# Kernel tuning notes

Measured on AMD Instinct MI355X. Metric: run time of the kernel, lower is better.

## Reference

```python
import jax, jax.numpy as jnp
import numpy as np

D_MODEL, N_HEADS, D_STATE, N_GROUPS, CHUNK = 2048, 32, 64, 1, 256
BATCH, SEQLEN = 2, 4096


def setup_inputs() -> dict:
    key = jax.random.key(0)
    ks = jax.random.split(key, 8)
    s = 0.02
    d, h, n, g = D_MODEL, N_HEADS, D_STATE, N_GROUPS
    return {
        "x": jax.random.normal(ks[0], (BATCH, SEQLEN, d), jnp.float32),
        "A_log": jnp.log(jnp.arange(1, h + 1, dtype=jnp.float32)),
        "D": jnp.ones((h,), jnp.float32),
        "B_w": jax.random.normal(ks[1], (g * n, d), jnp.float32) * s,
        "B_b": jnp.zeros((g * n,), jnp.float32),
        "C_w": jax.random.normal(ks[2], (g * n, d), jnp.float32) * s,
        "C_b": jnp.zeros((g * n,), jnp.float32),
        "dt_w": jax.random.normal(ks[3], (h, d), jnp.float32) * s,
        "dt_b": jnp.zeros((h,), jnp.float32),
        "out_w": jax.random.normal(ks[4], (d, d), jnp.float32) * s,
        "out_b": jnp.zeros((d,), jnp.float32),
    }


def segsum(v):
    # v: [..., T] -> [..., T, T]; out[i,j] = sum_{k=j+1..i} v[k] for i>=j, -inf else
    cs = jnp.cumsum(v, axis=-1)
    seg = cs[..., :, None] - cs[..., None, :]
    T = v.shape[-1]
    mask = jnp.tril(jnp.ones((T, T), bool))
    return jnp.where(mask, seg, -jnp.inf)


def _ssd(x, A_log, D, B_w, B_b, C_w, C_b, dt_w, dt_b, out_w, out_b):
    b, t, d = x.shape
    h = A_log.shape[0]
    n = B_w.shape[0] // N_GROUPS
    p = d // h
    l = CHUNK
    c = t // l

    A = -jnp.exp(A_log.astype(jnp.float32))                      # [h]
    B = (x @ B_w.T + B_b).reshape(b, t, N_GROUPS, n)             # g=1
    C = (x @ C_w.T + C_b).reshape(b, t, N_GROUPS, n)
    B = jnp.broadcast_to(B, (b, t, h, n))                        # repeat groups -> heads
    C = jnp.broadcast_to(C, (b, t, h, n))
    dt = jax.nn.softplus(x @ dt_w.T + dt_b)                      # [b,t,h]
    xh = x.reshape(b, t, h, p)

    # chunked SSD (Mamba2 mamba_chunk_scan_combined math)
    xc = xh.reshape(b, c, l, h, p)
    Bc = B.reshape(b, c, l, h, n)
    Cc = C.reshape(b, c, l, h, n)
    dtc = dt.reshape(b, c, l, h)
    dA = jnp.transpose(dtc * A, (0, 3, 1, 2))                    # [b,h,c,l]
    A_cumsum = jnp.cumsum(dA, axis=-1)                           # [b,h,c,l]

    # 1. intra-chunk (diagonal blocks)
    L = jnp.exp(segsum(dA))                                      # [b,h,c,l,l]
    xdt = xc * dtc[..., None]                                    # [b,c,l,h,p]
    Y_diag = jnp.einsum('bclhn,bcshn,bhcls,bcshp->bclhp', Cc, Bc, L, xdt)

    # 2. per-chunk final states
    decay_states = jnp.exp(A_cumsum[..., -1:] - A_cumsum)        # [b,h,c,l]
    states = jnp.einsum('bclhn,bhcl,bclhp->bchpn', Bc, decay_states, xdt)

    # 3. inter-chunk recurrence on chunk states
    states = jnp.concatenate([jnp.zeros_like(states[:, :1]), states], axis=1)  # [b,c+1,h,p,n]
    dA_last = jnp.pad(A_cumsum[..., -1], ((0, 0), (0, 0), (1, 0)))             # [b,h,c+1]
    decay_chunk = jnp.exp(segsum(dA_last))                                     # [b,h,c+1,c+1]
    new_states = jnp.einsum('bhzc,bchpn->bzhpn', decay_chunk, states)
    prev_states = new_states[:, :-1]                                           # [b,c,h,p,n]

    # 4. state -> output contribution
    state_decay_out = jnp.exp(A_cumsum)                          # [b,h,c,l]
    Y_off = jnp.einsum('bclhn,bchpn,bhcl->bclhp', Cc, prev_states, state_decay_out)

    Y = (Y_diag + Y_off).reshape(b, t, h, p) + D[None, None, :, None] * xh
    return Y.reshape(b, t, d) @ out_w.T + out_b


def reference(x, A_log, D, B_w, B_b, C_w, C_b, dt_w, dt_b, out_w, out_b):
    return _ssd(x, A_log, D, B_w, B_b, C_w, C_b, dt_w, dt_b, out_w, out_b)
```

## Files before the change

kernel.cpp:

```cpp
#include <hip/hip_runtime.h>
#include <hip/hip_bf16.h>
#include <math.h>

namespace {
constexpr int kDModel = 2048;
constexpr int kHeads  = 32;
constexpr int kState  = 64;
constexpr int kP      = 64;
constexpr int kChunk  = 256;
constexpr int kNChunk = 16;
constexpr int kBatch  = 2;
constexpr int kSeq    = 4096;
constexpr int kM      = kBatch * kSeq;
}

typedef __bf16 bf16_t;
typedef __attribute__((ext_vector_type(8))) __bf16 bf16x8;
typedef __attribute__((ext_vector_type(4))) __bf16 bf16x4;
typedef __attribute__((ext_vector_type(4))) float f32x4;

__device__ __forceinline__ void gload_lds16(const void* g, void* l) {
    __builtin_amdgcn_global_load_lds(
        (const __attribute__((address_space(1))) void*)g,
        (__attribute__((address_space(3))) void*)l,
        16, 0, 0);
}

__global__ __launch_bounds__(256)
void gemm_bcdt(const bf16_t* __restrict__ A, const bf16_t* __restrict__ W,
               const float* __restrict__ b0, const float* __restrict__ b1,
               const float* __restrict__ b2,
               bf16_t* __restrict__ o0h, bf16_t* __restrict__ o1h,
               float* __restrict__ o2f)
{
    constexpr int K = kDModel;
    __shared__ __bf16 AstS[64 * 32];
    __shared__ __bf16 WstS[128 * 32];
    const int tid  = threadIdx.x;
    const int lane = tid & 63;
    const int wave = tid >> 6;
    const int wm = (wave >> 1) * 32;
    const int wn = (wave & 1) * 64;
    const int l15 = lane & 15, quad = lane >> 4;
    const int m0 = blockIdx.y * 64;
    const int n0 = blockIdx.x * 128;
    const int u0 = tid, u1 = tid + 256;

    f32x4 acc[2][4];
    #pragma unroll
    for (int i = 0; i < 2; ++i)
        #pragma unroll
        for (int j = 0; j < 4; ++j)
            acc[i][j] = (f32x4){0.f, 0.f, 0.f, 0.f};

    for (int k0 = 0; k0 < K; k0 += 32) {
        gload_lds16(A + (size_t)(m0 + (tid >> 2)) * K + k0 + (tid & 3) * 8, AstS + tid * 8);
        gload_lds16(W + (size_t)(n0 + (u0 >> 2)) * K + k0 + (u0 & 3) * 8, WstS + u0 * 8);
        gload_lds16(W + (size_t)(n0 + (u1 >> 2)) * K + k0 + (u1 & 3) * 8, WstS + u1 * 8);
        __syncthreads();
        bf16x8 af[2], bfr[4];
        #pragma unroll
        for (int mi = 0; mi < 2; ++mi)
            af[mi] = *reinterpret_cast<const bf16x8*>(&AstS[(wm + mi * 16 + l15) * 32 + quad * 8]);
        #pragma unroll
        for (int ni = 0; ni < 4; ++ni)
            bfr[ni] = *reinterpret_cast<const bf16x8*>(&WstS[(wn + ni * 16 + l15) * 32 + quad * 8]);
        #pragma unroll
        for (int mi = 0; mi < 2; ++mi)
            #pragma unroll
            for (int ni = 0; ni < 4; ++ni)
                acc[mi][ni] = __builtin_amdgcn_mfma_f32_16x16x32_bf16(
                    af[mi], bfr[ni], acc[mi][ni], 0, 0, 0);
        __syncthreads();
    }

    #pragma unroll
    for (int mi = 0; mi < 2; ++mi) {
        #pragma unroll
        for (int reg = 0; reg < 4; ++reg) {
            const int r = m0 + wm + mi * 16 + quad * 4 + reg;
            #pragma unroll
            for (int ni = 0; ni < 4; ++ni) {
                const float v = acc[mi][ni][reg];
                const int n = n0 + wn + ni * 16 + l15;
                if (n < 64) {
                    o0h[(size_t)r * 64 + n] = (bf16_t)(v + b0[n]);
                } else if (n < 128) {
                    o1h[(size_t)r * 64 + (n - 64)] = (bf16_t)(v + b1[n - 64]);
                } else if (n < 160) {
                    float z = v + b2[n - 128];
                    o2f[(size_t)r * 32 + (n - 128)] = (z > 20.f) ? z : log1pf(expf(z));
                }
            }
        }
    }
}

__global__ __launch_bounds__(512, 2)
void gemm256_out(const bf16_t* __restrict__ Ap, const bf16_t* __restrict__ Bp,
                 const float* __restrict__ bias, float* __restrict__ C)
{
    constexpr int M = 8192, N = 2048, NT = 2048 / 32;
    __shared__ __bf16 Ab[3][4 * 256 * 8];
    __shared__ __bf16 Bb[3][4 * 256 * 8];
    const int tid  = threadIdx.x;
    const int lane = tid & 63;
    const int wave = tid >> 6;
    const int l15 = lane & 15, quad = lane >> 4;
    const int bid = blockIdx.x;
    const int mt = (bid & 7) * 4 + ((bid >> 3) & 3);
    const int nt = bid >> 5;
    const int m0 = mt * 256;
    const int n0 = nt * 256;
    const int wm = (wave >> 2) * 128;
    const int wn = (wave & 3) * 64;

    const int u0 = tid, u1 = tid + 512;
    auto stage = [&](int t2, int stb) {
        const int ks0 = t2 * 4;
        const bf16_t* As = Ap + ((size_t)ks0 * M + m0) * 8;
        const bf16_t* Bs = Bp + ((size_t)ks0 * N + n0) * 8;
        __bf16* Al = &Ab[stb][0];
        __bf16* Bl = &Bb[stb][0];
        gload_lds16(As + ((size_t)(u0 >> 8) * M + (u0 & 255)) * 8, Al + u0 * 8);
        gload_lds16(As + ((size_t)(u1 >> 8) * M + (u1 & 255)) * 8, Al + u1 * 8);
        gload_lds16(Bs + ((size_t)(u0 >> 8) * N + (u0 & 255)) * 8, Bl + u0 * 8);
        gload_lds16(Bs + ((size_t)(u1 >> 8) * N + (u1 & 255)) * 8, Bl + u1 * 8);
    };

    f32x4 acc[8][4];
    #pragma unroll
    for (int i = 0; i < 8; ++i)
        #pragma unroll
        for (int j = 0; j < 4; ++j)
            acc[i][j] = (f32x4){0.f, 0.f, 0.f, 0.f};

    stage(0, 0);
    stage(1, 1);
    asm volatile("s_waitcnt vmcnt(4)" ::: "memory");
    __builtin_amdgcn_s_barrier();

    int cur = 0;
    for (int t = 0; t < NT; ++t) {
        const __bf16* Ac = &Ab[cur][0];
        const __bf16* Bc = &Bb[cur][0];
        int stb = cur + 2; if (stb >= 3) stb -= 3;

        bf16x8 af[4], bfr[4];
        #pragma unroll
        for (int mi = 0; mi < 4; ++mi)
            af[mi] = *reinterpret_cast<const bf16x8*>(
                &Ac[(quad * 256 + wm + mi * 16 + l15) * 8]);
        #pragma unroll
        for (int nj = 0; nj < 4; ++nj)
            bfr[nj] = *reinterpret_cast<const bf16x8*>(
                &Bc[(quad * 256 + wn + nj * 16 + l15) * 8]);
        if (t < NT - 2) stage(t + 2, stb);
        __builtin_amdgcn_s_setprio(1);
        #pragma unroll
        for (int mi = 0; mi < 4; ++mi)
            #pragma unroll
            for (int nj = 0; nj < 4; ++nj)
                acc[mi][nj] = __builtin_amdgcn_mfma_f32_16x16x32_bf16(
                    af[mi], bfr[nj], acc[mi][nj], 0, 0, 0);
        __builtin_amdgcn_s_setprio(0);

        #pragma unroll
        for (int mi = 0; mi < 4; ++mi)
            af[mi] = *reinterpret_cast<const bf16x8*>(
                &Ac[(quad * 256 + wm + 64 + mi * 16 + l15) * 8]);
        __builtin_amdgcn_s_setprio(1);
        #pragma unroll
        for (int mi = 0; mi < 4; ++mi)
            #pragma unroll
            for (int nj = 0; nj < 4; ++nj)
                acc[4 + mi][nj] = __builtin_amdgcn_mfma_f32_16x16x32_bf16(
                    af[mi], bfr[nj], acc[4 + mi][nj], 0, 0, 0);
        __builtin_amdgcn_s_setprio(0);

        if (t < NT - 2) {
            asm volatile("s_waitcnt vmcnt(4)" ::: "memory");
        } else if (t < NT - 1) {
            asm volatile("s_waitcnt vmcnt(0)" ::: "memory");
        }
        if (t < NT - 1) __builtin_amdgcn_s_barrier();
        cur = cur + 1; if (cur == 3) cur = 0;
    }

    float bia[4];
    #pragma unroll
    for (int nj = 0; nj < 4; ++nj) bia[nj] = bias[n0 + wn + nj * 16 + l15];
    #pragma unroll
    for (int mi = 0; mi < 8; ++mi) {
        #pragma unroll
        for (int reg = 0; reg < 4; ++reg) {
            const int r = m0 + wm + mi * 16 + quad * 4 + reg;
            #pragma unroll
            for (int nj = 0; nj < 4; ++nj) {
                const int c = n0 + wn + nj * 16 + l15;
                C[(size_t)r * N + c] = acc[mi][nj][reg] + bia[nj];
            }
        }
    }
}

__global__ __launch_bounds__(256)
void cvt_bf16_kernel(const float* __restrict__ src, bf16_t* __restrict__ dst, int n)
{
    const int i = (blockIdx.x * 256 + threadIdx.x) * 4;
    if (i + 3 < n) {
        const float4 v = *reinterpret_cast<const float4*>(src + i);
        dst[i + 0] = (bf16_t)v.x;
        dst[i + 1] = (bf16_t)v.y;
        dst[i + 2] = (bf16_t)v.z;
        dst[i + 3] = (bf16_t)v.w;
    }
}

__global__ __launch_bounds__(256)
void pack_wob_kernel(const float* __restrict__ W, bf16_t* __restrict__ Wp)
{
    const int idx = blockIdx.x * 256 + threadIdx.x;
    const int n = idx >> 8, ks = idx & 255;
    const float4 v0 = *reinterpret_cast<const float4*>(W + (size_t)n * 2048 + ks * 8);
    const float4 v1 = *reinterpret_cast<const float4*>(W + (size_t)n * 2048 + ks * 8 + 4);
    bf16x8 o;
    o[0] = (__bf16)v0.x; o[1] = (__bf16)v0.y; o[2] = (__bf16)v0.z; o[3] = (__bf16)v0.w;
    o[4] = (__bf16)v1.x; o[5] = (__bf16)v1.y; o[6] = (__bf16)v1.z; o[7] = (__bf16)v1.w;
    *reinterpret_cast<bf16x8*>(Wp + ((size_t)ks * 2048 + n) * 8) = o;
}

__global__ __launch_bounds__(256)
void pack_w_kernel(const float* __restrict__ B_w, const float* __restrict__ C_w,
                   const float* __restrict__ dt_w, bf16_t* __restrict__ wcat)
{
    const int idx = blockIdx.x * 256 + threadIdx.x;
    const int r = idx >> 11, k = idx & 2047;
    float v = 0.f;
    if (r < 64)       v = B_w[r * 2048 + k];
    else if (r < 128) v = C_w[(r - 64) * 2048 + k];
    else if (r < 160) v = dt_w[(r - 128) * 2048 + k];
    wcat[idx] = (bf16_t)v;
}

__global__ __launch_bounds__(kChunk)
void dtcumsum_kernel(const float* __restrict__ dtm, const float* __restrict__ A_log,
                     float* __restrict__ Acs)
{
    const int blk = blockIdx.x;
    const int ci = blk & (kNChunk - 1);
    const int hi = (blk >> 4) & (kHeads - 1);
    const int bi = blk >> 9;
    const int t = threadIdx.x;
    const float Ah = -expf(A_log[hi]);
    __shared__ float s[kChunk];
    s[t] = dtm[((size_t)bi * kSeq + ci * kChunk + t) * kHeads + hi] * Ah;
    __syncthreads();
    for (int off = 1; off < kChunk; off <<= 1) {
        const float add = (t >= off) ? s[t - off] : 0.f;
        __syncthreads();
        s[t] += add;
        __syncthreads();
    }
    Acs[((size_t)(bi * kHeads + hi) * kNChunk + ci) * kChunk + t] = s[t];
}

__global__ __launch_bounds__(256)
void bT_kernel(const bf16_t* __restrict__ Bb16, bf16_t* __restrict__ bTg)
{
    const int ci = blockIdx.x & (kNChunk - 1);
    const int bi = blockIdx.x >> 4;
    const size_t rowbase = (size_t)bi * kSeq + ci * kChunk;
    __shared__ __bf16 T[64 * 264];
    const int tid = threadIdx.x;
    bf16x8 v[8];
    #pragma unroll
    for (int e = 0; e < 8; ++e)
        v[e] = *reinterpret_cast<const bf16x8*>(Bb16 + (rowbase + tid) * 64 + e * 8);
    #pragma unroll
    for (int e = 0; e < 8; ++e)
        #pragma unroll
        for (int j = 0; j < 8; ++j)
            T[(e * 8 + j) * 264 + tid] = v[e][j];
    __syncthreads();
    const int n = tid >> 2, seg = (tid & 3) * 64;
    bf16_t* dst = bTg + ((size_t)(bi * kNChunk + ci)) * (64 * 256) + n * 256 + seg;
    #pragma unroll
    for (int j = 0; j < 8; ++j) {
        *reinterpret_cast<bf16x8*>(dst + j * 8) =
            *reinterpret_cast<const bf16x8*>(&T[n * 264 + seg + j * 8]);
    }
}

__global__ __launch_bounds__(256)
void xdtT_kernel(const bf16_t* __restrict__ xb, const float* __restrict__ dtm,
                 bf16_t* __restrict__ xdtT)
{
    const int blk = blockIdx.x;
    const int hi = blk & (kHeads - 1);
    const int ci = (blk >> 5) & (kNChunk - 1);
    const int bi = blk >> 9;
    const size_t rowbase = (size_t)bi * kSeq + ci * kChunk;
    __shared__ __bf16 T[64 * 264];
    const int tid = threadIdx.x;
    const float d = dtm[(rowbase + tid) * kHeads + hi];
    bf16x8 v[8];
    #pragma unroll
    for (int e = 0; e < 8; ++e)
        v[e] = *reinterpret_cast<const bf16x8*>(xb + (rowbase + tid) * kDModel + hi * kP + e * 8);
    #pragma unroll
    for (int e = 0; e < 8; ++e)
        #pragma unroll
        for (int j = 0; j < 8; ++j)
            T[(e * 8 + j) * 264 + tid] = (__bf16)((float)v[e][j] * d);
    __syncthreads();
    const int p = tid >> 2, seg = (tid & 3) * 64;
    bf16_t* dst = xdtT + (size_t)blk * (64 * 256) + p * 256 + seg;
    #pragma unroll
    for (int j = 0; j < 8; ++j) {
        *reinterpret_cast<bf16x8*>(dst + j * 8) =
            *reinterpret_cast<const bf16x8*>(&T[p * 264 + seg + j * 8]);
    }
}

__global__ __launch_bounds__(256)
void states_mfma(const bf16_t* __restrict__ xdtT, const bf16_t* __restrict__ bTg,
                 const float* __restrict__ Acs, float* __restrict__ states)
{
    const int blk = blockIdx.x;
    const int hi = blk & (kHeads - 1);
    const int ci = (blk >> 5) & (kNChunk - 1);
    const int bi = blk >> 9;
    __shared__ __bf16 Xa[64 * 264];
    __shared__ __bf16 Bt[64 * 264];
    __shared__ float dec[kChunk];
    const int tid = threadIdx.x;
    const int lane = tid & 63;
    const int wave = tid >> 6;
    const int l15 = lane & 15, quad = lane >> 4;

    const float* acs = Acs + ((size_t)(bi * kHeads + hi) * kNChunk + ci) * kChunk;
    dec[tid] = expf(acs[kChunk - 1] - acs[tid]);
    __syncthreads();

    const bf16_t* bsrc = bTg + ((size_t)(bi * kNChunk + ci)) * (64 * 256);
    const bf16_t* xsrc = xdtT + (size_t)blk * (64 * 256);
    #pragma unroll
    for (int e = 0; e < 8; ++e) {
        const int u = e * 256 + tid;
        const int r = u >> 5, seg = (u & 31) * 8;
        *reinterpret_cast<bf16x8*>(&Bt[r * 264 + seg]) =
            *reinterpret_cast<const bf16x8*>(bsrc + r * 256 + seg);
        bf16x8 xv = *reinterpret_cast<const bf16x8*>(xsrc + r * 256 + seg);
        bf16x8 xo;
        #pragma unroll
        for (int j = 0; j < 8; ++j)
            xo[j] = (__bf16)((float)xv[j] * dec[seg + j]);
        *reinterpret_cast<bf16x8*>(&Xa[r * 264 + seg]) = xo;
    }
    __syncthreads();

    f32x4 acc[4];
    #pragma unroll
    for (int ni = 0; ni < 4; ++ni) acc[ni] = (f32x4){0.f, 0.f, 0.f, 0.f};
    #pragma unroll
    for (int kk = 0; kk < 8; ++kk) {
        const bf16x8 af = *reinterpret_cast<const bf16x8*>(
            &Xa[(wave * 16 + l15) * 264 + kk * 32 + quad * 8]);
        #pragma unroll
        for (int ni = 0; ni < 4; ++ni) {
            const bf16x8 bf = *reinterpret_cast<const bf16x8*>(
                &Bt[(ni * 16 + l15) * 264 + kk * 32 + quad * 8]);
            acc[ni] = __builtin_amdgcn_mfma_f32_16x16x32_bf16(af, bf, acc[ni], 0, 0, 0);
        }
    }
    float* sp = states + (size_t)blk * (kP * kState);
    #pragma unroll
    for (int reg = 0; reg < 4; ++reg) {
        const int p = wave * 16 + quad * 4 + reg;
        #pragma unroll
        for (int ni = 0; ni < 4; ++ni)
            sp[(size_t)p * kState + ni * 16 + l15] = acc[ni][reg];
    }
}

__global__ __launch_bounds__(256)
void chunkscan_kernel(const float* __restrict__ states, const float* __restrict__ Acs,
                      float* __restrict__ prevs)
{
    const int q  = blockIdx.x & 15;
    const int hi = (blockIdx.x >> 4) & (kHeads - 1);
    const int bi = blockIdx.x >> 9;
    const int e  = q * 256 + threadIdx.x;
    __shared__ float ea[kNChunk];
    if (threadIdx.x < kNChunk)
        ea[threadIdx.x] = expf(Acs[((size_t)(bi * kHeads + hi) * kNChunk + threadIdx.x)
                                   * kChunk + kChunk - 1]);
    __syncthreads();
    float P = 0.f;
    prevs[((size_t)(bi * kNChunk + 0) * kHeads + hi) * (kP * kState) + e] = 0.f;
    for (int c = 1; c < kNChunk; ++c) {
        P = fmaf(ea[c - 1], P,
                 states[((size_t)(bi * kNChunk + (c - 1)) * kHeads + hi) * (kP * kState) + e]);
        prevs[((size_t)(bi * kNChunk + c) * kHeads + hi) * (kP * kState) + e] = P;
    }
}

__global__ __launch_bounds__(256)
void ychunk_mfma(const float* __restrict__ x, const bf16_t* __restrict__ Bb16,
                 const bf16_t* __restrict__ Cb16, const bf16_t* __restrict__ xdtT,
                 const float* __restrict__ Acs, const float* __restrict__ prevs,
                 const float* __restrict__ Dvec, bf16_t* __restrict__ Yp)
{
    const int blk = blockIdx.x;
    const int lt = blk & 3;
    const int hi = (blk >> 2) & (kHeads - 1);
    const int ci = (blk >> 7) & (kNChunk - 1);
    const int bi = blk >> 11;
    __shared__ float acs_s[kChunk];
    __shared__ __bf16 Cs[64 * 72];
    __shared__ __bf16 Bs[64 * 72];
    __shared__ __bf16 Xt[64 * 72];
    __shared__ __bf16 Sp[64 * 72];
    const int tid = threadIdx.x;
    const int lane = tid & 63;
    const int wave = tid >> 6;
    const int l15 = lane & 15, quad = lane >> 4;
    const size_t rowbase = (size_t)bi * kSeq + ci * kChunk;
    const bf16_t* xdsrc = xdtT + ((size_t)((bi * kNChunk + ci) * kHeads + hi)) * (64 * 256);

    acs_s[tid] = Acs[((size_t)(bi * kHeads + hi) * kNChunk + ci) * kChunk + tid];
    #pragma unroll
    for (int e = 0; e < 2; ++e) {
        const int u = e * 256 + tid;
        const int r = u >> 3, seg = (u & 7) * 8;
        *reinterpret_cast<bf16x8*>(&Cs[r * 72 + seg]) =
            *reinterpret_cast<const bf16x8*>(Cb16 + (rowbase + lt * 64 + r) * 64 + seg);
    }
    const float* pp = prevs + ((size_t)(bi * kNChunk + ci) * kHeads + hi) * (kP * kState);
    #pragma unroll
    for (int e = 0; e < 4; ++e) {
        const int idx = e * 1024 + tid * 4;
        const int r = idx >> 6, c = idx & 63;
        const float4 vp = *reinterpret_cast<const float4*>(pp + idx);
        bf16x4 p4;
        p4[0] = (__bf16)vp.x; p4[1] = (__bf16)vp.y;
        p4[2] = (__bf16)vp.z; p4[3] = (__bf16)vp.w;
        *reinterpret_cast<bf16x4*>(&Bs[r * 72 + c]) = p4;
    }
    __syncthreads();

    bf16x8 af[2];
    af[0] = *reinterpret_cast<const bf16x8*>(&Cs[(wave * 16 + l15) * 72 + quad * 8]);
    af[1] = *reinterpret_cast<const bf16x8*>(&Cs[(wave * 16 + l15) * 72 + 32 + quad * 8]);

    f32x4 yacc[4];
    #pragma unroll
    for (int ni = 0; ni < 4; ++ni) yacc[ni] = (f32x4){0.f, 0.f, 0.f, 0.f};
    #pragma unroll
    for (int ni = 0; ni < 4; ++ni) {
        const bf16x8 b0 = *reinterpret_cast<const bf16x8*>(&Bs[(ni * 16 + l15) * 72 + quad * 8]);
        const bf16x8 b1 = *reinterpret_cast<const bf16x8*>(&Bs[(ni * 16 + l15) * 72 + 32 + quad * 8]);
        yacc[ni] = __builtin_amdgcn_mfma_f32_16x16x32_bf16(af[0], b0, yacc[ni], 0, 0, 0);
        yacc[ni] = __builtin_amdgcn_mfma_f32_16x16x32_bf16(af[1], b1, yacc[ni], 0, 0, 0);
    }
    const int mrow = wave * 16 + quad * 4;
    {
        float es[4];
        #pragma unroll
        for (int reg = 0; reg < 4; ++reg) es[reg] = expf(acs_s[lt * 64 + mrow + reg]);
        #pragma unroll
        for (int ni = 0; ni < 4; ++ni)
            #pragma unroll
            for (int reg = 0; reg < 4; ++reg) yacc[ni][reg] *= es[reg];
    }

    for (int st = 0; st <= lt; ++st) {
        __syncthreads();
        #pragma unroll
        for (int e = 0; e < 2; ++e) {
            const int u = e * 256 + tid;
            const int r = u >> 3, seg = (u & 7) * 8;
            *reinterpret_cast<bf16x8*>(&Bs[r * 72 + seg]) =
                *reinterpret_cast<const bf16x8*>(Bb16 + (rowbase + st * 64 + r) * 64 + seg);
            *reinterpret_cast<bf16x8*>(&Xt[r * 72 + seg]) =
                *reinterpret_cast<const bf16x8*>(xdsrc + r * 256 + st * 64 + seg);
        }
        __syncthreads();
        f32x4 sacc[4];
        #pragma unroll
        for (int ni = 0; ni < 4; ++ni) sacc[ni] = (f32x4){0.f, 0.f, 0.f, 0.f};
        #pragma unroll
        for (int ni = 0; ni < 4; ++ni) {
            const bf16x8 b0 = *reinterpret_cast<const bf16x8*>(&Bs[(ni * 16 + l15) * 72 + quad * 8]);
            const bf16x8 b1 = *reinterpret_cast<const bf16x8*>(&Bs[(ni * 16 + l15) * 72 + 32 + quad * 8]);
            sacc[ni] = __builtin_amdgcn_mfma_f32_16x16x32_bf16(af[0], b0, sacc[ni], 0, 0, 0);
            sacc[ni] = __builtin_amdgcn_mfma_f32_16x16x32_bf16(af[1], b1, sacc[ni], 0, 0, 0);
        }
        #pragma unroll
        for (int reg = 0; reg < 4; ++reg) {
            const int l = lt * 64 + mrow + reg;
            const float al = acs_s[l];
            #pragma unroll
            for (int ni = 0; ni < 4; ++ni) {
                const int scol = ni * 16 + l15;
                const int sg = st * 64 + scol;
                float v = sacc[ni][reg] * expf(al - acs_s[sg]);
                if (st == lt && sg > l) v = 0.f;
                Sp[(mrow + reg) * 72 + scol] = (__bf16)v;
            }
        }
        __syncthreads();
        const bf16x8 as0 = *reinterpret_cast<const bf16x8*>(&Sp[(wave * 16 + l15) * 72 + quad * 8]);
        const bf16x8 as1 = *reinterpret_cast<const bf16x8*>(&Sp[(wave * 16 + l15) * 72 + 32 + quad * 8]);
        #pragma unroll
        for (int ni = 0; ni < 4; ++ni) {
            const bf16x8 x0 = *reinterpret_cast<const bf16x8*>(&Xt[(ni * 16 + l15) * 72 + quad * 8]);
            const bf16x8 x1 = *reinterpret_cast<const bf16x8*>(&Xt[(ni * 16 + l15) * 72 + 32 + quad * 8]);
            yacc[ni] = __builtin_amdgcn_mfma_f32_16x16x32_bf16(as0, x0, yacc[ni], 0, 0, 0);
            yacc[ni] = __builtin_amdgcn_mfma_f32_16x16x32_bf16(as1, x1, yacc[ni], 0, 0, 0);
        }
    }

    const float Dh = Dvec[hi];
    #pragma unroll
    for (int reg = 0; reg < 4; ++reg) {
        const size_t tg = rowbase + lt * 64 + mrow + reg;
        #pragma unroll
        for (int ni = 0; ni < 4; ++ni) {
            const int p = ni * 16 + l15;
            const float v = yacc[ni][reg] + Dh * x[tg * kDModel + hi * kP + p];
            Yp[((size_t)(hi * 8 + (p >> 3)) * (size_t)kM + tg) * 8 + (p & 7)] = (bf16_t)v;
        }
    }
}

extern "C" void kernel_launch(void* const* d_in, const int* in_sizes, int n_in,
                              void* d_out, int out_size, void* d_ws, size_t ws_size,
                              hipStream_t stream)
{
    (void)in_sizes; (void)n_in; (void)out_size; (void)ws_size;
    const float* x     = (const float*)d_in[0];
    const float* A_log = (const float*)d_in[1];
    const float* Dvec  = (const float*)d_in[2];
    const float* B_w   = (const float*)d_in[3];
    const float* B_b   = (const float*)d_in[4];
    const float* C_w   = (const float*)d_in[5];
    const float* C_b   = (const float*)d_in[6];
    const float* dt_w  = (const float*)d_in[7];
    const float* dt_b  = (const float*)d_in[8];
    const float* out_w = (const float*)d_in[9];
    const float* out_b = (const float*)d_in[10];
    float* out = (float*)d_out;

    float* ws = (float*)d_ws;
    float* dtm    = ws;
    float* Acs    = dtm + (size_t)kM * kHeads;
    float* states = Acs + (size_t)kBatch * kHeads * kNChunk * kChunk;
    float* prevs  = states + (size_t)kBatch * kNChunk * kHeads * kP * kState;
    bf16_t* xb    = (bf16_t*)(prevs + (size_t)kBatch * kNChunk * kHeads * kP * kState);
    bf16_t* Y     = xb;
    bf16_t* Bb16  = xb + (size_t)kM * kDModel;
    bf16_t* Cb16  = Bb16 + (size_t)kM * kState;
    bf16_t* xdtT  = Cb16 + (size_t)kM * kState;
    bf16_t* bTg   = xdtT + (size_t)kM * kDModel;
    bf16_t* wcat  = bTg + (size_t)kBatch * kNChunk * kState * kChunk;
    bf16_t* wob   = wcat + (size_t)256 * kDModel;

    const dim3 blk(256);
    cvt_bf16_kernel<<<dim3(kM * kDModel / 1024), blk, 0, stream>>>(x, xb, kM * kDModel);
    pack_wob_kernel<<<dim3(kDModel * 256 / 256), blk, 0, stream>>>(out_w, wob);
    pack_w_kernel<<<dim3(256 * kDModel / 256), blk, 0, stream>>>(B_w, C_w, dt_w, wcat);
    gemm_bcdt<<<dim3(2, kM / 64), blk, 0, stream>>>(xb, wcat,
                                                    B_b, C_b, dt_b,
                                                    Bb16, Cb16, dtm);
    dtcumsum_kernel<<<dim3(kBatch * kHeads * kNChunk), dim3(kChunk), 0, stream>>>(dtm, A_log, Acs);
    bT_kernel<<<dim3(kBatch * kNChunk), blk, 0, stream>>>(Bb16, bTg);
    xdtT_kernel<<<dim3(kBatch * kNChunk * kHeads), blk, 0, stream>>>(xb, dtm, xdtT);
    states_mfma<<<dim3(kBatch * kNChunk * kHeads), blk, 0, stream>>>(xdtT, bTg, Acs, states);
    chunkscan_kernel<<<dim3(kBatch * kHeads * 16), blk, 0, stream>>>(states, Acs, prevs);
    ychunk_mfma<<<dim3(kBatch * kNChunk * kHeads * 4), blk, 0, stream>>>(
        x, Bb16, Cb16, xdtT, Acs, prevs, Dvec, Y);
    gemm256_out<<<dim3(256), dim3(512), 0, stream>>>(Y, wob, out_b, out);
}
```

Before: 351.9 us.

## Use 32x32 MFMA in out GEMM, merge ychunk row tiles, store prev states bf16

```diff
diff --git a/kernel.cpp b/kernel.cpp
--- a/kernel.cpp
+++ b/kernel.cpp
@@ -18,6 +18,7 @@
 typedef __attribute__((ext_vector_type(8))) __bf16 bf16x8;
 typedef __attribute__((ext_vector_type(4))) __bf16 bf16x4;
 typedef __attribute__((ext_vector_type(4))) float f32x4;
+typedef __attribute__((ext_vector_type(16))) float f32x16;
 
 __device__ __forceinline__ void gload_lds16(const void* g, void* l) {
     __builtin_amdgcn_global_load_lds(
@@ -106,7 +107,7 @@
     const int tid  = threadIdx.x;
     const int lane = tid & 63;
     const int wave = tid >> 6;
-    const int l15 = lane & 15, quad = lane >> 4;
+    const int row32 = lane & 31, half = lane >> 5;
     const int bid = blockIdx.x;
     const int mt = (bid & 7) * 4 + ((bid >> 3) & 3);
     const int nt = bid >> 5;
@@ -128,12 +129,14 @@
         gload_lds16(Bs + ((size_t)(u1 >> 8) * N + (u1 & 255)) * 8, Bl + u1 * 8);
     };
 
-    f32x4 acc[8][4];
-    #pragma unroll
-    for (int i = 0; i < 8; ++i)
-        #pragma unroll
-        for (int j = 0; j < 4; ++j)
-            acc[i][j] = (f32x4){0.f, 0.f, 0.f, 0.f};
+    f32x16 acc[4][2];
+    #pragma unroll
+    for (int i = 0; i < 4; ++i)
+        #pragma unroll
+        for (int j = 0; j < 2; ++j)
+            #pragma unroll
+            for (int e = 0; e < 16; ++e)
+                acc[i][j][e] = 0.f;
 
     stage(0, 0);
     stage(1, 1);
@@ -146,36 +149,40 @@
         const __bf16* Bc = &Bb[cur][0];
         int stb = cur + 2; if (stb >= 3) stb -= 3;
 
-        bf16x8 af[4], bfr[4];
-        #pragma unroll
-        for (int mi = 0; mi < 4; ++mi)
-            af[mi] = *reinterpret_cast<const bf16x8*>(
-                &Ac[(quad * 256 + wm + mi * 16 + l15) * 8]);
-        #pragma unroll
-        for (int nj = 0; nj < 4; ++nj)
-            bfr[nj] = *reinterpret_cast<const bf16x8*>(
-                &Bc[(quad * 256 + wn + nj * 16 + l15) * 8]);
+        bf16x8 af[4], bfr[2];
+        #pragma unroll
+        for (int mf = 0; mf < 4; ++mf)
+            af[mf] = *reinterpret_cast<const bf16x8*>(
+                &Ac[(half * 256 + wm + mf * 32 + row32) * 8]);
+        #pragma unroll
+        for (int nf = 0; nf < 2; ++nf)
+            bfr[nf] = *reinterpret_cast<const bf16x8*>(
+                &Bc[(half * 256 + wn + nf * 32 + row32) * 8]);
         if (t < NT - 2) stage(t + 2, stb);
         __builtin_amdgcn_s_setprio(1);
         #pragma unroll
-        for (int mi = 0; mi < 4; ++mi)
-            #pragma unroll
-            for (int nj = 0; nj < 4; ++nj)
-                acc[mi][nj] = __builtin_amdgcn_mfma_f32_16x16x32_bf16(
-                    af[mi], bfr[nj], acc[mi][nj], 0, 0, 0);
+        for (int mf = 0; mf < 4; ++mf)
+            #pragma unroll
+            for (int nf = 0; nf < 2; ++nf)
+                acc[mf][nf] = __builtin_amdgcn_mfma_f32_32x32x16_bf16(
+                    af[mf], bfr[nf], acc[mf][nf], 0, 0, 0);
         __builtin_amdgcn_s_setprio(0);
 
         #pragma unroll
-        for (int mi = 0; mi < 4; ++mi)
-            af[mi] = *reinterpret_cast<const bf16x8*>(
-                &Ac[(quad * 256 + wm + 64 + mi * 16 + l15) * 8]);
+        for (int mf = 0; mf < 4; ++mf)
+            af[mf] = *reinterpret_cast<const bf16x8*>(
+                &Ac[((2 + half) * 256 + wm + mf * 32 + row32) * 8]);
+        #pragma unroll
+        for (int nf = 0; nf < 2; ++nf)
+            bfr[nf] = *reinterpret_cast<const bf16x8*>(
+                &Bc[((2 + half) * 256 + wn + nf * 32 + row32) * 8]);
         __builtin_amdgcn_s_setprio(1);
         #pragma unroll
-        for (int mi = 0; mi < 4; ++mi)
-            #pragma unroll
-            for (int nj = 0; nj < 4; ++nj)
-                acc[4 + mi][nj] = __builtin_amdgcn_mfma_f32_16x16x32_bf16(
-                    af[mi], bfr[nj], acc[4 + mi][nj], 0, 0, 0);
+        for (int mf = 0; mf < 4; ++mf)
+            #pragma unroll
+            for (int nf = 0; nf < 2; ++nf)
+                acc[mf][nf] = __builtin_amdgcn_mfma_f32_32x32x16_bf16(
+                    af[mf], bfr[nf], acc[mf][nf], 0, 0, 0);
         __builtin_amdgcn_s_setprio(0);
 
         if (t < NT - 2) {
@@ -187,18 +194,18 @@
         cur = cur + 1; if (cur == 3) cur = 0;
     }
 
-    float bia[4];
-    #pragma unroll
-    for (int nj = 0; nj < 4; ++nj) bia[nj] = bias[n0 + wn + nj * 16 + l15];
-    #pragma unroll
-    for (int mi = 0; mi < 8; ++mi) {
-        #pragma unroll
-        for (int reg = 0; reg < 4; ++reg) {
-            const int r = m0 + wm + mi * 16 + quad * 4 + reg;
-            #pragma unroll
-            for (int nj = 0; nj < 4; ++nj) {
-                const int c = n0 + wn + nj * 16 + l15;
-                C[(size_t)r * N + c] = acc[mi][nj][reg] + bia[nj];
+    float bia[2];
+    #pragma unroll
+    for (int nf = 0; nf < 2; ++nf) bia[nf] = bias[n0 + wn + nf * 32 + row32];
+    #pragma unroll
+    for (int mf = 0; mf < 4; ++mf) {
+        #pragma unroll
+        for (int nf = 0; nf < 2; ++nf) {
+            #pragma unroll
+            for (int reg = 0; reg < 16; ++reg) {
+                const int r = m0 + wm + mf * 32 + (reg & 3) + 8 * (reg >> 2) + 4 * half;
+                const int c = n0 + wn + nf * 32 + row32;
+                C[(size_t)r * N + c] = acc[mf][nf][reg] + bia[nf];
             }
         }
     }
@@ -386,7 +393,7 @@
 
 __global__ __launch_bounds__(256)
 void chunkscan_kernel(const float* __restrict__ states, const float* __restrict__ Acs,
-                      float* __restrict__ prevs)
+                      bf16_t* __restrict__ prevsb)
 {
     const int q  = blockIdx.x & 15;
     const int hi = (blockIdx.x >> 4) & (kHeads - 1);
@@ -398,27 +405,28 @@
                                    * kChunk + kChunk - 1]);
     __syncthreads();
     float P = 0.f;
-    prevs[((size_t)(bi * kNChunk + 0) * kHeads + hi) * (kP * kState) + e] = 0.f;
+    prevsb[((size_t)(bi * kNChunk + 0) * kHeads + hi) * (kP * kState) + e] = (bf16_t)0.f;
     for (int c = 1; c < kNChunk; ++c) {
         P = fmaf(ea[c - 1], P,
                  states[((size_t)(bi * kNChunk + (c - 1)) * kHeads + hi) * (kP * kState) + e]);
-        prevs[((size_t)(bi * kNChunk + c) * kHeads + hi) * (kP * kState) + e] = P;
-    }
-}
-
-__global__ __launch_bounds__(256)
-void ychunk_mfma(const float* __restrict__ x, const bf16_t* __restrict__ Bb16,
-                 const bf16_t* __restrict__ Cb16, const bf16_t* __restrict__ xdtT,
-                 const float* __restrict__ Acs, const float* __restrict__ prevs,
+        prevsb[((size_t)(bi * kNChunk + c) * kHeads + hi) * (kP * kState) + e] = (bf16_t)P;
+    }
+}
+
+__global__ __launch_bounds__(256)
+void ychunk_mfma(const bf16_t* __restrict__ Bb16, const bf16_t* __restrict__ Cb16,
+                 const bf16_t* __restrict__ xdtT, const float* __restrict__ Acs,
+                 const bf16_t* __restrict__ prevsb, const float* __restrict__ dtm,
                  const float* __restrict__ Dvec, bf16_t* __restrict__ Yp)
 {
     const int blk = blockIdx.x;
-    const int lt = blk & 3;
-    const int hi = (blk >> 2) & (kHeads - 1);
-    const int ci = (blk >> 7) & (kNChunk - 1);
-    const int bi = blk >> 11;
+    const int hi = blk & (kHeads - 1);
+    const int ci = (blk >> 5) & (kNChunk - 1);
+    const int bi = blk >> 9;
     __shared__ float acs_s[kChunk];
-    __shared__ __bf16 Cs[64 * 72];
+    __shared__ float dts[kChunk];
+    __shared__ __bf16 Cs[256 * 72];
+    __shared__ __bf16 Ps[64 * 72];
     __shared__ __bf16 Bs[64 * 72];
     __shared__ __bf16 Xt[64 * 72];
     __shared__ __bf16 Sp[64 * 72];
@@ -426,56 +434,56 @@
     const int lane = tid & 63;
     const int wave = tid >> 6;
     const int l15 = lane & 15, quad = lane >> 4;
+    const int mrow = wave * 16 + quad * 4;
     const size_t rowbase = (size_t)bi * kSeq + ci * kChunk;
-    const bf16_t* xdsrc = xdtT + ((size_t)((bi * kNChunk + ci) * kHeads + hi)) * (64 * 256);
+    const bf16_t* xdsrc = xdtT + (size_t)blk * (64 * 256);
 
     acs_s[tid] = Acs[((size_t)(bi * kHeads + hi) * kNChunk + ci) * kChunk + tid];
+    dts[tid]   = dtm[(rowbase + tid) * kHeads + hi];
+    #pragma unroll
+    for (int e = 0; e < 8; ++e) {
+        const int u = e * 256 + tid;
+        const int r = u >> 3, seg = (u & 7) * 8;
+        *reinterpret_cast<bf16x8*>(&Cs[r * 72 + seg]) =
+            *reinterpret_cast<const bf16x8*>(Cb16 + (rowbase + r) * 64 + seg);
+    }
+    const bf16_t* pp = prevsb + ((size_t)(bi * kNChunk + ci) * kHeads + hi) * (kP * kState);
     #pragma unroll
     for (int e = 0; e < 2; ++e) {
         const int u = e * 256 + tid;
         const int r = u >> 3, seg = (u & 7) * 8;
-        *reinterpret_cast<bf16x8*>(&Cs[r * 72 + seg]) =
-            *reinterpret_cast<const bf16x8*>(Cb16 + (rowbase + lt * 64 + r) * 64 + seg);
-    }
-    const float* pp = prevs + ((size_t)(bi * kNChunk + ci) * kHeads + hi) * (kP * kState);
-    #pragma unroll
-    for (int e = 0; e < 4; ++e) {
-        const int idx = e * 1024 + tid * 4;
-        const int r = idx >> 6, c = idx & 63;
-        const float4 vp = *reinterpret_cast<const float4*>(pp + idx);
-        bf16x4 p4;
-        p4[0] = (__bf16)vp.x; p4[1] = (__bf16)vp.y;
-        p4[2] = (__bf16)vp.z; p4[3] = (__bf16)vp.w;
-        *reinterpret_cast<bf16x4*>(&Bs[r * 72 + c]) = p4;
+        *reinterpret_cast<bf16x8*>(&Ps[r * 72 + seg]) =
+            *reinterpret_cast<const bf16x8*>(pp + r * 64 + seg);
     }
     __syncthreads();
 
-    bf16x8 af[2];
-    af[0] = *reinterpret_cast<const bf16x8*>(&Cs[(wave * 16 + l15) * 72 + quad * 8]);
-    af[1] = *reinterpret_cast<const bf16x8*>(&Cs[(wave * 16 + l15) * 72 + 32 + quad * 8]);
-
-    f32x4 yacc[4];
-    #pragma unroll
-    for (int ni = 0; ni < 4; ++ni) yacc[ni] = (f32x4){0.f, 0.f, 0.f, 0.f};
-    #pragma unroll
-    for (int ni = 0; ni < 4; ++ni) {
-        const bf16x8 b0 = *reinterpret_cast<const bf16x8*>(&Bs[(ni * 16 + l15) * 72 + quad * 8]);
-        const bf16x8 b1 = *reinterpret_cast<const bf16x8*>(&Bs[(ni * 16 + l15) * 72 + 32 + quad * 8]);
-        yacc[ni] = __builtin_amdgcn_mfma_f32_16x16x32_bf16(af[0], b0, yacc[ni], 0, 0, 0);
-        yacc[ni] = __builtin_amdgcn_mfma_f32_16x16x32_bf16(af[1], b1, yacc[ni], 0, 0, 0);
-    }
-    const int mrow = wave * 16 + quad * 4;
-    {
+    f32x4 yacc[4][4];
+    #pragma unroll
+    for (int lt = 0; lt < 4; ++lt) {
+        #pragma unroll
+        for (int ni = 0; ni < 4; ++ni) yacc[lt][ni] = (f32x4){0.f, 0.f, 0.f, 0.f};
+        const bf16x8 af0 = *reinterpret_cast<const bf16x8*>(
+            &Cs[(lt * 64 + wave * 16 + l15) * 72 + quad * 8]);
+        const bf16x8 af1 = *reinterpret_cast<const bf16x8*>(
+            &Cs[(lt * 64 + wave * 16 + l15) * 72 + 32 + quad * 8]);
+        #pragma unroll
+        for (int ni = 0; ni < 4; ++ni) {
+            const bf16x8 b0 = *reinterpret_cast<const bf16x8*>(&Ps[(ni * 16 + l15) * 72 + quad * 8]);
+            const bf16x8 b1 = *reinterpret_cast<const bf16x8*>(&Ps[(ni * 16 + l15) * 72 + 32 + quad * 8]);
+            yacc[lt][ni] = __builtin_amdgcn_mfma_f32_16x16x32_bf16(af0, b0, yacc[lt][ni], 0, 0, 0);
+            yacc[lt][ni] = __builtin_amdgcn_mfma_f32_16x16x32_bf16(af1, b1, yacc[lt][ni], 0, 0, 0);
+        }
         float es[4];
         #pragma unroll
         for (int reg = 0; reg < 4; ++reg) es[reg] = expf(acs_s[lt * 64 + mrow + reg]);
         #pragma unroll
         for (int ni = 0; ni < 4; ++ni)
             #pragma unroll
-            for (int reg = 0; reg < 4; ++reg) yacc[ni][reg] *= es[reg];
-    }
-
-    for (int st = 0; st <= lt; ++st) {
+            for (int reg = 0; reg < 4; ++reg) yacc[lt][ni][reg] *= es[reg];
+    }
+
+    const float Dh = Dvec[hi];
+    for (int st = 0; st < 4; ++st) {
         __syncthreads();
         #pragma unroll
         for (int e = 0; e < 2; ++e) {
@@ -487,50 +495,62 @@
                 *reinterpret_cast<const bf16x8*>(xdsrc + r * 256 + st * 64 + seg);
         }
         __syncthreads();
-        f32x4 sacc[4];
-        #pragma unroll
-        for (int ni = 0; ni < 4; ++ni) sacc[ni] = (f32x4){0.f, 0.f, 0.f, 0.f};
-        #pragma unroll
-        for (int ni = 0; ni < 4; ++ni) {
-            const bf16x8 b0 = *reinterpret_cast<const bf16x8*>(&Bs[(ni * 16 + l15) * 72 + quad * 8]);
-            const bf16x8 b1 = *reinterpret_cast<const bf16x8*>(&Bs[(ni * 16 + l15) * 72 + 32 + quad * 8]);
-            sacc[ni] = __builtin_amdgcn_mfma_f32_16x16x32_bf16(af[0], b0, sacc[ni], 0, 0, 0);
-            sacc[ni] = __builtin_amdgcn_mfma_f32_16x16x32_bf16(af[1], b1, sacc[ni], 0, 0, 0);
-        }
-        #pragma unroll
-        for (int reg = 0; reg < 4; ++reg) {
-            const int l = lt * 64 + mrow + reg;
-            const float al = acs_s[l];
+        #pragma unroll
+        for (int lt = 0; lt < 4; ++lt) {
+            if (lt < st) continue;
+            const bf16x8 af0 = *reinterpret_cast<const bf16x8*>(
+                &Cs[(lt * 64 + wave * 16 + l15) * 72 + quad * 8]);
+            const bf16x8 af1 = *reinterpret_cast<const bf16x8*>(
+                &Cs[(lt * 64 + wave * 16 + l15) * 72 + 32 + quad * 8]);
+            f32x4 sacc[4];
+            #pragma unroll
+            for (int ni = 0; ni < 4; ++ni) sacc[ni] = (f32x4){0.f, 0.f, 0.f, 0.f};
             #pragma unroll
             for (int ni = 0; ni < 4; ++ni) {
-                const int scol = ni * 16 + l15;
-                const int sg = st * 64 + scol;
-                float v = sacc[ni][reg] * expf(al - acs_s[sg]);
-                if (st == lt && sg > l) v = 0.f;
-                Sp[(mrow + reg) * 72 + scol] = (__bf16)v;
+                const bf16x8 b0 = *reinterpret_cast<const bf16x8*>(&Bs[(ni * 16 + l15) * 72 + quad * 8]);
+                const bf16x8 b1 = *reinterpret_cast<const bf16x8*>(&Bs[(ni * 16 + l15) * 72 + 32 + quad * 8]);
+                sacc[ni] = __builtin_amdgcn_mfma_f32_16x16x32_bf16(af0, b0, sacc[ni], 0, 0, 0);
+                sacc[ni] = __builtin_amdgcn_mfma_f32_16x16x32_bf16(af1, b1, sacc[ni], 0, 0, 0);
             }
-        }
-        __syncthreads();
-        const bf16x8 as0 = *reinterpret_cast<const bf16x8*>(&Sp[(wave * 16 + l15) * 72 + quad * 8]);
-        const bf16x8 as1 = *reinterpret_cast<const bf16x8*>(&Sp[(wave * 16 + l15) * 72 + 32 + quad * 8]);
-        #pragma unroll
-        for (int ni = 0; ni < 4; ++ni) {
-            const bf16x8 x0 = *reinterpret_cast<const bf16x8*>(&Xt[(ni * 16 + l15) * 72 + quad * 8]);
-            const bf16x8 x1 = *reinterpret_cast<const bf16x8*>(&Xt[(ni * 16 + l15) * 72 + 32 + quad * 8]);
-            yacc[ni] = __builtin_amdgcn_mfma_f32_16x16x32_bf16(as0, x0, yacc[ni], 0, 0, 0);
-            yacc[ni] = __builtin_amdgcn_mfma_f32_16x16x32_bf16(as1, x1, yacc[ni], 0, 0, 0);
-        }
-    }
-
-    const float Dh = Dvec[hi];
-    #pragma unroll
-    for (int reg = 0; reg < 4; ++reg) {
-        const size_t tg = rowbase + lt * 64 + mrow + reg;
-        #pragma unroll
-        for (int ni = 0; ni < 4; ++ni) {
-            const int p = ni * 16 + l15;
-            const float v = yacc[ni][reg] + Dh * x[tg * kDModel + hi * kP + p];
-            Yp[((size_t)(hi * 8 + (p >> 3)) * (size_t)kM + tg) * 8 + (p & 7)] = (bf16_t)v;
+            #pragma unroll
+            for (int reg = 0; reg < 4; ++reg) {
+                const int l = lt * 64 + mrow + reg;
+                const float al = acs_s[l];
+                #pragma unroll
+                for (int ni = 0; ni < 4; ++ni) {
+                    const int scol = ni * 16 + l15;
+                    const int sg = st * 64 + scol;
+                    float v = sacc[ni][reg] * expf(al - acs_s[sg]);
+                    if (st == lt && sg > l) v = 0.f;
+                    Sp[(mrow + reg) * 72 + scol] = (__bf16)v;
+                }
+            }
+            __syncthreads();
+            const bf16x8 as0 = *reinterpret_cast<const bf16x8*>(&Sp[(wave * 16 + l15) * 72 + quad * 8]);
+            const bf16x8 as1 = *reinterpret_cast<const bf16x8*>(&Sp[(wave * 16 + l15) * 72 + 32 + quad * 8]);
+            #pragma unroll
+            for (int ni = 0; ni < 4; ++ni) {
+                const bf16x8 x0 = *reinterpret_cast<const bf16x8*>(&Xt[(ni * 16 + l15) * 72 + quad * 8]);
+                const bf16x8 x1 = *reinterpret_cast<const bf16x8*>(&Xt[(ni * 16 + l15) * 72 + 32 + quad * 8]);
+                yacc[lt][ni] = __builtin_amdgcn_mfma_f32_16x16x32_bf16(as0, x0, yacc[lt][ni], 0, 0, 0);
+                yacc[lt][ni] = __builtin_amdgcn_mfma_f32_16x16x32_bf16(as1, x1, yacc[lt][ni], 0, 0, 0);
+            }
+            if (lt == st) {
+                #pragma unroll
+                for (int reg = 0; reg < 4; ++reg) {
+                    const int lrow = mrow + reg;
+                    const size_t tg = rowbase + lt * 64 + lrow;
+                    const float dinv = 1.f / dts[lt * 64 + lrow];
+                    #pragma unroll
+                    for (int ni = 0; ni < 4; ++ni) {
+                        const int p = ni * 16 + l15;
+                        const float xv = (float)Xt[p * 72 + lrow] * dinv;
+                        const float v = yacc[lt][ni][reg] + Dh * xv;
+                        Yp[((size_t)(hi * 8 + (p >> 3)) * (size_t)kM + tg) * 8 + (p & 7)] = (bf16_t)v;
+                    }
+                }
+            }
+            __syncthreads();
         }
     }
 }
@@ -557,8 +577,8 @@
     float* dtm    = ws;
     float* Acs    = dtm + (size_t)kM * kHeads;
     float* states = Acs + (size_t)kBatch * kHeads * kNChunk * kChunk;
-    float* prevs  = states + (size_t)kBatch * kNChunk * kHeads * kP * kState;
-    bf16_t* xb    = (bf16_t*)(prevs + (size_t)kBatch * kNChunk * kHeads * kP * kState);
+    bf16_t* prevsb = (bf16_t*)(states + (size_t)kBatch * kNChunk * kHeads * kP * kState);
+    bf16_t* xb    = prevsb + (size_t)kBatch * kNChunk * kHeads * kP * kState;
     bf16_t* Y     = xb;
     bf16_t* Bb16  = xb + (size_t)kM * kDModel;
     bf16_t* Cb16  = Bb16 + (size_t)kM * kState;
@@ -571,15 +591,14 @@
     cvt_bf16_kernel<<<dim3(kM * kDModel / 1024), blk, 0, stream>>>(x, xb, kM * kDModel);
     pack_wob_kernel<<<dim3(kDModel * 256 / 256), blk, 0, stream>>>(out_w, wob);
     pack_w_kernel<<<dim3(256 * kDModel / 256), blk, 0, stream>>>(B_w, C_w, dt_w, wcat);
-    gemm_bcdt<<<dim3(2, kM / 64), blk, 0, stream>>>(xb, wcat,
-                                                    B_b, C_b, dt_b,
+    gemm_bcdt<<<dim3(2, kM / 64), blk, 0, stream>>>(xb, wcat, B_b, C_b, dt_b,
                                                     Bb16, Cb16, dtm);
     dtcumsum_kernel<<<dim3(kBatch * kHeads * kNChunk), dim3(kChunk), 0, stream>>>(dtm, A_log, Acs);
     bT_kernel<<<dim3(kBatch * kNChunk), blk, 0, stream>>>(Bb16, bTg);
     xdtT_kernel<<<dim3(kBatch * kNChunk * kHeads), blk, 0, stream>>>(xb, dtm, xdtT);
     states_mfma<<<dim3(kBatch * kNChunk * kHeads), blk, 0, stream>>>(xdtT, bTg, Acs, states);
-    chunkscan_kernel<<<dim3(kBatch * kHeads * 16), blk, 0, stream>>>(states, Acs, prevs);
-    ychunk_mfma<<<dim3(kBatch * kNChunk * kHeads * 4), blk, 0, stream>>>(
-        x, Bb16, Cb16, xdtT, Acs, prevs, Dvec, Y);
+    chunkscan_kernel<<<dim3(kBatch * kHeads * 16), blk, 0, stream>>>(states, Acs, prevsb);
+    ychunk_mfma<<<dim3(kBatch * kNChunk * kHeads), blk, 0, stream>>>(
+        Bb16, Cb16, xdtT, Acs, prevsb, dtm, Dvec, Y);
     gemm256_out<<<dim3(256), dim3(512), 0, stream>>>(Y, wob, out_b, out);
 }
```

New measurement: 383.5 us. 1.09x slower.
